# Kernel tuning notes

Measured on AMD Instinct MI355X. Metric: run time of the kernel, lower is better.

The kernel has to match this reference:

```python
import jax, jax.numpy as jnp
import numpy as np

N_NODES = 100000
N_EDGES = 800000
IN_DIM, HID, OUT_DIM = 128, 96, 32
BN_EPS = 1e-5


def gcn_conv(x, W, b, src, dst, n):
    # PyG GCNConv: linear -> symmetric-normalized aggregation (with self-loops) -> +bias
    h = x @ W  # [N, out]
    sl = jnp.arange(n)
    s = jnp.concatenate([src, sl])
    d = jnp.concatenate([dst, sl])
    deg = jax.ops.segment_sum(jnp.ones(s.shape[0], dtype=x.dtype), d, num_segments=n)
    dinv = jnp.where(deg > 0, jax.lax.rsqrt(deg), 0.0)
    norm = dinv[s] * dinv[d]  # [E+N]
    out = jax.ops.segment_sum(norm[:, None] * h[s], d, num_segments=n)
    return out + b


def batchnorm(x, gamma, beta):
    mu = jnp.mean(x, axis=0)
    var = jnp.var(x, axis=0)
    return gamma * (x - mu) * jax.lax.rsqrt(var + BN_EPS) + beta


def setup_inputs() -> dict:
    key = jax.random.key(0)
    ks = jax.random.split(key, 8)
    glorot = lambda k, fi, fo: jax.random.normal(k, (fi, fo), jnp.float32) * np.sqrt(2.0 / (fi + fo))
    return {
        "x": jax.random.normal(ks[0], (N_NODES, IN_DIM), jnp.float32),
        "edge_index": jax.random.randint(ks[1], (2, N_EDGES), 0, N_NODES, jnp.int64),
        "W1": glorot(ks[2], IN_DIM, HID), "b1": jnp.zeros((HID,), jnp.float32),
        "W2": glorot(ks[3], HID, HID), "b2": jnp.zeros((HID,), jnp.float32),
        "W3": glorot(ks[4], HID, OUT_DIM), "b3": jnp.zeros((OUT_DIM,), jnp.float32),
        "g1": jnp.ones((HID,), jnp.float32), "be1": jnp.zeros((HID,), jnp.float32),
        "g2": jnp.ones((HID,), jnp.float32), "be2": jnp.zeros((HID,), jnp.float32),
    }


def reference(x, edge_index, W1, b1, W2, b2, W3, b3, g1, be1, g2, be2):
    src, dst = edge_index[0], edge_index[1]
    n = x.shape[0]
    h = gcn_conv(x, W1, b1, src, dst, n)
    h = jax.nn.relu(batchnorm(h, g1, be1))  # dropout is identity in eval
    h = gcn_conv(h, W2, b2, src, dst, n)
    h = jax.nn.relu(batchnorm(h, g2, be2))
    h = gcn_conv(h, W3, b3, src, dst, n)
    return jax.nn.log_softmax(h, axis=-1)
```

## Files before the change

### kernel.cpp

```cpp
#include <hip/hip_runtime.h>
#include <hip/hip_fp16.h>
#include <cstddef>

#define NN 100000
#define NE 800000
#define DIN 128
#define HID 96
#define DOUT 32
static constexpr float BN_EPS = 1e-5f;
#define SCAN_NB ((NN + 255) / 256)

typedef unsigned short u16;
typedef unsigned int u32;

using f32x4 = __attribute__((ext_vector_type(4))) float;
using bf16x8 = __attribute__((ext_vector_type(8))) short;

__device__ __forceinline__ float b2f(u32 lo16) {
    union { u32 u; float f; } c; c.u = lo16 << 16; return c.f;
}
__device__ __forceinline__ u16 f2b(float f) {
    union { float f; u32 u; } c; c.f = f;
    return (u16)((c.u + 0x7FFFu + ((c.u >> 16) & 1u)) >> 16);
}
__device__ __forceinline__ u32 pack_edge(int s, float w) {
    __half h = __float2half(w);
    return ((u32)s << 15) | (u32)__half_as_ushort(h);
}
__device__ __forceinline__ int edge_src(u32 pk) { return (int)(pk >> 15); }
__device__ __forceinline__ float edge_wt(u32 pk) {
    return __half2float(__ushort_as_half((u16)(pk & 0x7FFFu)));
}


__global__ void k_init(int* __restrict__ deg) {
    int i = blockIdx.x * 256 + threadIdx.x;
    if (i < NN) deg[i] = 0;
}

__global__ __launch_bounds__(256) void k_wpack(const float* __restrict__ W1,
                                               const float* __restrict__ W2,
                                               const float* __restrict__ W3,
                                               u16* __restrict__ w1p,
                                               u16* __restrict__ w2p,
                                               u16* __restrict__ w3p) {
    int e = blockIdx.x * 256 + threadIdx.x;
    const float* W; u16* P; int N, nf, idx;
    if (e < 12288)      { W = W1; P = w1p; N = 96; nf = 24; idx = e; }
    else if (e < 21504) { W = W2; P = w2p; N = 96; nf = 18; idx = e - 12288; }
    else                { W = W3; P = w3p; N = 32; nf = 6;  idx = e - 21504; }
    int f = idx >> 9, r = idx & 511;
    int lane = r >> 3, j = r & 7;
    int CFT = N / 16;
    int kt = f / CFT, c = f % CFT;
    int k = kt * 32 + (lane >> 4) * 8 + j;
    int col = c * 16 + (lane & 15);
    float v = W[k * N + col];
    u16 hi = f2b(v);
    u16 lo = f2b(v - b2f(hi));
    P[idx] = hi;
    P[nf * 512 + idx] = lo;
}

__global__ __launch_bounds__(256) void k_scan1(const int* __restrict__ deg,
                                               int* __restrict__ row_start,
                                               int* __restrict__ blksum,
                                               float* __restrict__ dinv) {
    __shared__ int lds[256];
    int t = threadIdx.x;
    int i = blockIdx.x * 256 + t;
    int v = (i < NN) ? deg[i] : 0;
    if (i < NN) dinv[i] = rsqrtf((float)(v + 1));
    lds[t] = v;
    __syncthreads();
#pragma unroll
    for (int off = 1; off < 256; off <<= 1) {
        int add = (t >= off) ? lds[t - off] : 0;
        __syncthreads();
        lds[t] += add;
        __syncthreads();
    }
    if (i < NN) row_start[i] = lds[t] - v;
    if (t == 255) blksum[blockIdx.x] = lds[255];
}

__global__ __launch_bounds__(512) void k_scan2(int* __restrict__ blksum,
                                               int* __restrict__ row_start,
                                               float* __restrict__ meta) {
    __shared__ int lds[512];
    int t = threadIdx.x;
    if (t < 384) meta[t] = 0.f;
    int v = (t < SCAN_NB) ? blksum[t] : 0;
    lds[t] = v;
    __syncthreads();
#pragma unroll
    for (int off = 1; off < 512; off <<= 1) {
        int add = (t >= off) ? lds[t - off] : 0;
        __syncthreads();
        lds[t] += add;
        __syncthreads();
    }
    if (t < SCAN_NB) blksum[t] = lds[t] - v;
    if (t == 511) row_start[NN] = lds[511];
}

__global__ __launch_bounds__(256) void k_scan3(int* __restrict__ row_start,
                                               const int* __restrict__ blksum) {
    int i = blockIdx.x * 256 + threadIdx.x;
    if (i < NN) row_start[i] += blksum[blockIdx.x];
}

__global__ void k_scatter(const int* __restrict__ src, const int* __restrict__ dst,
                          const int* __restrict__ row_start,
                          const int* __restrict__ rank,
                          const float* __restrict__ dinv,
                          u32* __restrict__ ewt) {
    int e = blockIdx.x * blockDim.x + threadIdx.x;
    if (e < NE) {
        int d = dst[e];
        int p = row_start[d] + rank[e];
        int s = src[e];
        ewt[p] = pack_edge(s, dinv[s]);
    }
}

template <int K, int N, bool FUSE, typename XT>
__device__ __forceinline__ void gemmM_body(int bid, const XT* __restrict__ X,
                                           const u16* __restrict__ Wp,
                                           u16* __restrict__ Z,
                                           const float* __restrict__ bnA,
                                           const float* __restrict__ bnC, int M) {
    constexpr int KT = K / 32;
    constexpr int CFT = N / 16;
    constexpr int WN = (N == 96) ? 2 : 1;
    constexpr int WM = 4 / WN;
    constexpr int CF = CFT / WN;
    constexpr int RF = 64 / (WM * 16);
    constexpr int XSB = K + 8;
    __shared__ u16 Ah[64 * XSB];
    __shared__ u16 Al[64 * XSB];
    __shared__ float As[FUSE ? K : 1], Cs[FUSE ? K : 1];

    int tid = threadIdx.x;
    if (FUSE) {
        if (tid < K) { As[tid] = bnA[tid]; Cs[tid] = bnC[tid]; }
        __syncthreads();
    }
    int row0 = bid * 64;
    int sr = tid >> 2, sq = tid & 3;
    int grow = row0 + sr;
    if constexpr (sizeof(XT) == 4) {
#pragma unroll
        for (int i = 0; i < 8; ++i) {
            int c0 = sq * 32 + i * 4;
            float4 v = make_float4(0.f, 0.f, 0.f, 0.f);
            if (grow < M) v = *(const float4*)&X[(size_t)grow * K + c0];
            float vv[4] = {v.x, v.y, v.z, v.w};
            u32 hpk[2], lpk[2];
#pragma unroll
            for (int p = 0; p < 2; ++p) {
                u16 h0 = f2b(vv[2 * p]), h1 = f2b(vv[2 * p + 1]);
                u16 l0 = f2b(vv[2 * p] - b2f(h0));
                u16 l1 = f2b(vv[2 * p + 1] - b2f(h1));
                hpk[p] = (u32)h0 | ((u32)h1 << 16);
                lpk[p] = (u32)l0 | ((u32)l1 << 16);
            }
            *(uint2*)&Ah[sr * XSB + c0] = make_uint2(hpk[0], hpk[1]);
            *(uint2*)&Al[sr * XSB + c0] = make_uint2(lpk[0], lpk[1]);
        }
    } else {
#pragma unroll
        for (int i = 0; i < 3; ++i) {
            int c0 = sq * 24 + i * 8;
            uint4 v = make_uint4(0, 0, 0, 0);
            if (grow < M) v = *(const uint4*)&X[(size_t)grow * K + c0];
            u32 w[4] = {v.x, v.y, v.z, v.w};
            u32 hq[4], lq[4];
#pragma unroll
            for (int p = 0; p < 4; ++p) {
                float x0 = b2f(w[p] & 0xFFFFu);
                float x1 = b2f(w[p] >> 16);
                if (FUSE) {
                    x0 = fmaxf(fmaf(As[c0 + 2 * p], x0, Cs[c0 + 2 * p]), 0.f);
                    x1 = fmaxf(fmaf(As[c0 + 2 * p + 1], x1, Cs[c0 + 2 * p + 1]), 0.f);
                }
                u16 h0 = f2b(x0), h1 = f2b(x1);
                u16 l0 = f2b(x0 - b2f(h0)), l1 = f2b(x1 - b2f(h1));
                hq[p] = (u32)h0 | ((u32)h1 << 16);
                lq[p] = (u32)l0 | ((u32)l1 << 16);
            }
            *(uint4*)&Ah[sr * XSB + c0] = make_uint4(hq[0], hq[1], hq[2], hq[3]);
            *(uint4*)&Al[sr * XSB + c0] = make_uint4(lq[0], lq[1], lq[2], lq[3]);
        }
    }
    __syncthreads();

    int wid = tid >> 6, lane = tid & 63;
    int wm = wid & (WM - 1), wn = wid / WM;
    int lr = lane & 15, lg = lane >> 4;
    f32x4 acc[RF][CF];
#pragma unroll
    for (int a = 0; a < RF; ++a)
#pragma unroll
        for (int b = 0; b < CF; ++b) acc[a][b] = (f32x4){0.f, 0.f, 0.f, 0.f};

    const u16* WpLo = Wp + KT * CFT * 512;
#pragma unroll
    for (int kt = 0; kt < KT; ++kt) {
        bf16x8 ah[RF], al[RF];
#pragma unroll
        for (int rf = 0; rf < RF; ++rf) {
            int row = wm * (RF * 16) + rf * 16 + lr;
            ah[rf] = *(const bf16x8*)&Ah[row * XSB + kt * 32 + lg * 8];
            al[rf] = *(const bf16x8*)&Al[row * XSB + kt * 32 + lg * 8];
        }
#pragma unroll
        for (int cf = 0; cf < CF; ++cf) {
            int f = kt * CFT + wn * CF + cf;
            bf16x8 bh = *(const bf16x8*)&Wp[f * 512 + lane * 8];
            bf16x8 bl = *(const bf16x8*)&WpLo[f * 512 + lane * 8];
#pragma unroll
            for (int rf = 0; rf < RF; ++rf) {
                acc[rf][cf] = __builtin_amdgcn_mfma_f32_16x16x32_bf16(ah[rf], bh, acc[rf][cf], 0, 0, 0);
                acc[rf][cf] = __builtin_amdgcn_mfma_f32_16x16x32_bf16(al[rf], bh, acc[rf][cf], 0, 0, 0);
                acc[rf][cf] = __builtin_amdgcn_mfma_f32_16x16x32_bf16(ah[rf], bl, acc[rf][cf], 0, 0, 0);
            }
        }
    }
#pragma unroll
    for (int rf = 0; rf < RF; ++rf)
#pragma unroll
        for (int cf = 0; cf < CF; ++cf)
#pragma unroll
            for (int rr = 0; rr < 4; ++rr) {
                int gr = row0 + wm * (RF * 16) + rf * 16 + lg * 4 + rr;
                if (gr < M) {
                    int col = (wn * CF + cf) * 16 + lr;
                    Z[(size_t)gr * N + col] = f2b(acc[rf][cf][rr]);
                }
            }
}

template <int K, int N, bool FUSE, typename XT>
__global__ __launch_bounds__(256) void k_gemm(const XT* __restrict__ X,
                                              const u16* __restrict__ Wp,
                                              u16* __restrict__ Z,
                                              const float* __restrict__ bnA,
                                              const float* __restrict__ bnC, int M) {
    gemmM_body<K, N, FUSE, XT>(blockIdx.x, X, Wp, Z, bnA, bnC, M);
}

__global__ __launch_bounds__(256) void k_gemm1_hist(const float* __restrict__ X,
                                                    const u16* __restrict__ Wp,
                                                    u16* __restrict__ Z, int M,
                                                    int gemm_blocks,
                                                    const int* __restrict__ dst,
                                                    int* __restrict__ deg,
                                                    int* __restrict__ rank) {
    if ((int)blockIdx.x < gemm_blocks) {
        gemmM_body<DIN, HID, false, float>(blockIdx.x, X, Wp, Z, nullptr, nullptr, M);
    } else {
        int e = ((int)blockIdx.x - gemm_blocks) * 256 + (int)threadIdx.x;
        if (e < NE) rank[e] = atomicAdd(&deg[dst[e]], 1);
    }
}

#define ACC8(UB, W)                                                     \
    acc[0] = fmaf(W, b2f((UB).x & 0xFFFFu), acc[0]);                    \
    acc[1] = fmaf(W, b2f((UB).x >> 16), acc[1]);                        \
    acc[2] = fmaf(W, b2f((UB).y & 0xFFFFu), acc[2]);                    \
    acc[3] = fmaf(W, b2f((UB).y >> 16), acc[3]);                        \
    acc[4] = fmaf(W, b2f((UB).z & 0xFFFFu), acc[4]);                    \
    acc[5] = fmaf(W, b2f((UB).z >> 16), acc[5]);                        \
    acc[6] = fmaf(W, b2f((UB).w & 0xFFFFu), acc[6]);                    \
    acc[7] = fmaf(W, b2f((UB).w >> 16), acc[7]);

__global__ __launch_bounds__(256) void k_agg96(const u16* __restrict__ Z,
                                               u16* __restrict__ H,
                                               const float* __restrict__ bias,
                                               const int* __restrict__ row_start,
                                               const u32* __restrict__ ewt,
                                               const float* __restrict__ dinv,
                                               float* __restrict__ gsum,
                                               float* __restrict__ gsq) {
    __shared__ float ssum[96], ssq[96];
    int tid = threadIdx.x;
    if (tid < 96) { ssum[tid] = 0.f; ssq[tid] = 0.f; }
    __syncthreads();
    int wid = tid >> 6, lane = tid & 63;
    int r = lane >> 4;
    int jraw = lane & 15;
    int j = jraw < 12 ? jraw : 11;
    bool jact = jraw < 12;
    u32 j16 = (u32)j << 4;
    const char* zb = (const char*)Z;
    float bia[8];
#pragma unroll
    for (int k = 0; k < 8; ++k) bia[k] = bias[8 * j + k];
    float lsum[8], lsq[8];
#pragma unroll
    for (int k = 0; k < 8; ++k) { lsum[k] = 0.f; lsq[k] = 0.f; }
    const int S = gridDim.x * 4;

    int n = blockIdx.x * 4 + wid;
    int e0 = 0, e1 = 0;
    u32 pr = 0;
    if (n < NN) {
        e0 = row_start[n]; e1 = row_start[n + 1];
        if (e0 + lane < e1) pr = ewt[e0 + lane];
    }
    while (n < NN) {
        int n2 = n + S;
        int e0n = 0, e1n = 0;
        if (n2 < NN) { e0n = row_start[n2]; e1n = row_start[n2 + 1]; }
        u32 prn = 0;
        if (n2 < NN && e0n + lane < e1n) prn = ewt[e0n + lane];

        float dn = dinv[n];
        int m = e1 - e0;
        float acc[8];
        uint4 us4 = make_uint4(0, 0, 0, 0);
        if (r == 0) us4 = *(const uint4*)(zb + (u32)n * 192u + j16);
        if (r == 0) {
            acc[0] = dn * b2f(us4.x & 0xFFFFu); acc[1] = dn * b2f(us4.x >> 16);
            acc[2] = dn * b2f(us4.y & 0xFFFFu); acc[3] = dn * b2f(us4.y >> 16);
            acc[4] = dn * b2f(us4.z & 0xFFFFu); acc[5] = dn * b2f(us4.z >> 16);
            acc[6] = dn * b2f(us4.w & 0xFFFFu); acc[7] = dn * b2f(us4.w >> 16);
        } else {
#pragma unroll
            for (int k = 0; k < 8; ++k) acc[k] = 0.f;
        }

        if (m <= 16) {
            uint4 ub[4]; float wc[4];
            int nch = (m + 3) >> 2;
#pragma unroll
            for (int c = 0; c < 4; ++c) {
                if (c < nch) {
                    int e = 4 * c + r;
                    u32 pk = __shfl(pr, e < m ? e : 0);
                    wc[c] = (e < m) ? edge_wt(pk) : 0.f;
                    ub[c] = *(const uint4*)(zb + (pk >> 15) * 192u + j16);
                }
            }
#pragma unroll
            for (int c = 0; c < 4; ++c) {
                if (c < nch) { ACC8(ub[c], wc[c]); }
            }
        } else {
            for (int base = 0; base < m; base += 64) {
                u32 cw = pr;
                if (base) {
                    int idx = e0 + base + lane;
                    cw = (idx < e1) ? ewt[idx] : 0;
                }
                int lim = m - base; if (lim > 64) lim = 64;
                for (int c = 0; c < lim; c += 4) {
                    int e = c + r;
                    u32 pk = __shfl(cw, e < lim ? e : 0);
                    float w = (e < lim) ? edge_wt(pk) : 0.f;
                    uint4 ub = *(const uint4*)(zb + (pk >> 15) * 192u + j16);
                    ACC8(ub, w);
                }
            }
        }

#pragma unroll
        for (int k = 0; k < 8; ++k) {
            float v = acc[k];
            v += __shfl_xor(v, 16);
            v += __shfl_xor(v, 32);
            acc[k] = v;
        }
        if (r == 0 && jact) {
            float h[8];
#pragma unroll
            for (int k = 0; k < 8; ++k) {
                h[k] = fmaf(dn, acc[k], bia[k]);
                lsum[k] += h[k];
                lsq[k] = fmaf(h[k], h[k], lsq[k]);
            }
            uint4 o;
            o.x = (u32)f2b(h[0]) | ((u32)f2b(h[1]) << 16);
            o.y = (u32)f2b(h[2]) | ((u32)f2b(h[3]) << 16);
            o.z = (u32)f2b(h[4]) | ((u32)f2b(h[5]) << 16);
            o.w = (u32)f2b(h[6]) | ((u32)f2b(h[7]) << 16);
            *(uint4*)((char*)H + (u32)n * 192u + j16) = o;
        }
        n = n2; e0 = e0n; e1 = e1n; pr = prn;
    }
    if (r == 0 && jact) {
#pragma unroll
        for (int k = 0; k < 8; ++k) {
            atomicAdd(&ssum[8 * j + k], lsum[k]);
            atomicAdd(&ssq[8 * j + k], lsq[k]);
        }
    }
    __syncthreads();
    if (tid < 96) { atomicAdd(&gsum[tid], ssum[tid]); atomicAdd(&gsq[tid], ssq[tid]); }
}

__global__ void k_bncoef(const float* __restrict__ gsum, const float* __restrict__ gsq,
                         const float* __restrict__ g, const float* __restrict__ be,
                         float* __restrict__ bnA, float* __restrict__ bnC) {
    int c = threadIdx.x;
    if (c < 96) {
        float mean = gsum[c] * (1.f / NN);
        float var = gsq[c] * (1.f / NN) - mean * mean;
        float inv = rsqrtf(var + BN_EPS);
        float a = g[c] * inv;
        bnA[c] = a;
        bnC[c] = fmaf(-a, mean, be[c]);
    }
}

__global__ __launch_bounds__(256) void k_agg32_lsm(const u16* __restrict__ Z,
                                                   float* __restrict__ Out,
                                                   const float* __restrict__ bias,
                                                   const int* __restrict__ row_start,
                                                   const u32* __restrict__ ewt,
                                                   const float* __restrict__ dinv) {
    int tid = threadIdx.x;
    int wid = tid >> 6, lane = tid & 63;
    int g = lane >> 4, sl = lane & 15;
    const u32* zu = (const u32*)Z;
    float b0 = bias[2 * sl], b1 = bias[2 * sl + 1];
    int stride = gridDim.x * 16;
    for (int n0 = (blockIdx.x * 4 + wid) * 4; n0 < NN; n0 += stride) {
        int n = n0 + g;
        bool vn = n < NN;
        float dn = vn ? dinv[n] : 0.f;
        u32 uself = vn ? zu[(size_t)n * 16 + sl] : 0;
        float a0a = dn * b2f(uself & 0xFFFFu);
        float a1a = dn * b2f(uself >> 16);
        float a0b = 0.f, a1b = 0.f;
        int e0 = vn ? row_start[n] : 0, e1 = vn ? row_start[n + 1] : 0;
        for (int eb = e0; eb < e1; eb += 16) {
            int m = e1 - eb; if (m > 16) m = 16;
            int idx = eb + sl;
            u32 plv = (idx < e1) ? ewt[idx] : 0;
            u32 u_[16]; float w_[16];
#pragma unroll
            for (int q = 0; q < 16; ++q) {
                bool v = q < m;
                u32 pk = __shfl(plv, v ? q : 0, 16);
                w_[q] = v ? edge_wt(pk) : 0.f;
                u_[q] = zu[(size_t)edge_src(pk) * 16 + sl];
            }
#pragma unroll
            for (int q = 0; q < 16; q += 2) {
                a0a = fmaf(w_[q], b2f(u_[q] & 0xFFFFu), a0a);
                a1a = fmaf(w_[q], b2f(u_[q] >> 16), a1a);
                a0b = fmaf(w_[q + 1], b2f(u_[q + 1] & 0xFFFFu), a0b);
                a1b = fmaf(w_[q + 1], b2f(u_[q + 1] >> 16), a1b);
            }
        }
        float v0 = fmaf(dn, a0a + a0b, b0);
        float v1 = fmaf(dn, a1a + a1b, b1);
        float mx = fmaxf(v0, v1);
#pragma unroll
        for (int off = 8; off; off >>= 1) mx = fmaxf(mx, __shfl_xor(mx, off, 16));
        float ex = __expf(v0 - mx) + __expf(v1 - mx);
#pragma unroll
        for (int off = 8; off; off >>= 1) ex += __shfl_xor(ex, off, 16);
        float lse = mx + __logf(ex);
        if (vn) {
            float2 o = make_float2(v0 - lse, v1 - lse);
            *(float2*)&Out[(size_t)n * 32 + 2 * sl] = o;
        }
    }
}


extern "C" void kernel_launch(void* const* d_in, const int* in_sizes, int n_in,
                              void* d_out, int out_size, void* d_ws, size_t ws_size,
                              hipStream_t stream) {
    const float* x  = (const float*)d_in[0];
    const int* ei   = (const int*)d_in[1];
    const float* W1 = (const float*)d_in[2];
    const float* b1 = (const float*)d_in[3];
    const float* W2 = (const float*)d_in[4];
    const float* b2 = (const float*)d_in[5];
    const float* W3 = (const float*)d_in[6];
    const float* b3 = (const float*)d_in[7];
    const float* g1 = (const float*)d_in[8];
    const float* be1 = (const float*)d_in[9];
    const float* g2 = (const float*)d_in[10];
    const float* be2 = (const float*)d_in[11];
    float* out = (float*)d_out;

    const int* src = ei;
    const int* dst = ei + NE;

    char* p = (char*)d_ws;
    size_t off = 0;
    auto take = [&](size_t bytes) {
        char* r = p + off;
        off = (off + bytes + 255) & ~(size_t)255;
        return r;
    };
    float* dinv      = (float*)take(NN * 4);
    int*   deg       = (int*)take(NN * 4);
    int*   row_start = (int*)take((NN + 1) * 4);
    int*   blksum    = (int*)take(SCAN_NB * 4);
    int*   rank      = (int*)take((size_t)NE * 4);
    u32*   ewt       = (u32*)take((size_t)NE * 4);
    float* meta      = (float*)take(768 * 4);
    u16*   w1p       = (u16*)take(24 * 512 * 2 * 2);
    u16*   w2p       = (u16*)take(18 * 512 * 2 * 2);
    u16*   w3p       = (u16*)take(6 * 512 * 2 * 2);
    u16*   bufA      = (u16*)take((size_t)NN * HID * 2);
    u16*   bufB      = (u16*)take((size_t)NN * HID * 2);

    float* sum1 = meta + 0,   *sq1 = meta + 96;
    float* sum2 = meta + 192, *sq2 = meta + 288;
    float* bnA1 = meta + 384, *bnC1 = meta + 480;
    float* bnA2 = meta + 576, *bnC2 = meta + 672;

    const int EB = (NE + 255) / 256;
    const int VB = (NN + 255) / 256;
    const int MB = (NN + 63) / 64;
    const int AB = 2048;

    k_wpack<<<96, 256, 0, stream>>>(W1, W2, W3, w1p, w2p, w3p);
    k_init<<<VB, 256, 0, stream>>>(deg);
    k_gemm1_hist<<<MB + EB, 256, 0, stream>>>(x, w1p, bufA, NN, MB, dst, deg, rank);
    k_scan1<<<SCAN_NB, 256, 0, stream>>>(deg, row_start, blksum, dinv);
    k_scan2<<<1, 512, 0, stream>>>(blksum, row_start, meta);
    k_scan3<<<SCAN_NB, 256, 0, stream>>>(row_start, blksum);
    k_scatter<<<EB, 256, 0, stream>>>(src, dst, row_start, rank, dinv, ewt);

    k_agg96<<<AB, 256, 0, stream>>>(bufA, bufB, b1, row_start, ewt, dinv, sum1, sq1);
    k_bncoef<<<1, 128, 0, stream>>>(sum1, sq1, g1, be1, bnA1, bnC1);

    k_gemm<HID, HID, true, u16><<<MB, 256, 0, stream>>>(bufB, w2p, bufA, bnA1, bnC1, NN);
    k_agg96<<<AB, 256, 0, stream>>>(bufA, bufB, b2, row_start, ewt, dinv, sum2, sq2);
    k_bncoef<<<1, 128, 0, stream>>>(sum2, sq2, g2, be2, bnA2, bnC2);

    k_gemm<HID, DOUT, true, u16><<<MB, 256, 0, stream>>>(bufB, w3p, bufA, bnA2, bnC2, NN);
    k_agg32_lsm<<<AB, 256, 0, stream>>>(bufA, out, b3, row_start, ewt, dinv);

    (void)in_sizes; (void)n_in; (void)out_size; (void)ws_size;
}
```

Measured before the change: 384.6 us.

## Fold BN coefficient kernels into GEMMs, memset inits, restructure agg32 per-wave node

Removes the two single-block BN coefficient kernels and has each fused GEMM block compute the scale and shift from the global sums. Replaces the degree-init kernel and the meta zeroing with hipMemsetAsync calls. Rewrites the final aggregation plus log-softmax so one wave handles one node: 16 edge groups of 4 lanes each load 16-byte rows, then a cross-lane reduction follows. This cuts launch count and changes the gather pattern, at the cost of redundant coefficient math per block and more shuffle reductions.

```diff
diff --git a/kernel.cpp b/kernel.cpp
--- a/kernel.cpp
+++ b/kernel.cpp
@@ -32,11 +32,6 @@
     return __half2float(__ushort_as_half((u16)(pk & 0x7FFFu)));
 }
 
-
-__global__ void k_init(int* __restrict__ deg) {
-    int i = blockIdx.x * 256 + threadIdx.x;
-    if (i < NN) deg[i] = 0;
-}
 
 __global__ __launch_bounds__(256) void k_wpack(const float* __restrict__ W1,
                                                const float* __restrict__ W2,
@@ -85,11 +80,9 @@
 }
 
 __global__ __launch_bounds__(512) void k_scan2(int* __restrict__ blksum,
-                                               int* __restrict__ row_start,
-                                               float* __restrict__ meta) {
+                                               int* __restrict__ row_start) {
     __shared__ int lds[512];
     int t = threadIdx.x;
-    if (t < 384) meta[t] = 0.f;
     int v = (t < SCAN_NB) ? blksum[t] : 0;
     lds[t] = v;
     __syncthreads();
@@ -128,8 +121,10 @@
 __device__ __forceinline__ void gemmM_body(int bid, const XT* __restrict__ X,
                                            const u16* __restrict__ Wp,
                                            u16* __restrict__ Z,
-                                           const float* __restrict__ bnA,
-                                           const float* __restrict__ bnC, int M) {
+                                           const float* __restrict__ gsum,
+                                           const float* __restrict__ gsq,
+                                           const float* __restrict__ gam,
+                                           const float* __restrict__ bet, int M) {
     constexpr int KT = K / 32;
     constexpr int CFT = N / 16;
     constexpr int WN = (N == 96) ? 2 : 1;
@@ -143,7 +138,14 @@
 
     int tid = threadIdx.x;
     if (FUSE) {
-        if (tid < K) { As[tid] = bnA[tid]; Cs[tid] = bnC[tid]; }
+        if (tid < K) {
+            float mean = gsum[tid] * (1.f / NN);
+            float var = gsq[tid] * (1.f / NN) - mean * mean;
+            float inv = rsqrtf(var + BN_EPS);
+            float a = gam[tid] * inv;
+            As[tid] = a;
+            Cs[tid] = fmaf(-a, mean, bet[tid]);
+        }
         __syncthreads();
     }
     int row0 = bid * 64;
@@ -245,9 +247,11 @@
 __global__ __launch_bounds__(256) void k_gemm(const XT* __restrict__ X,
                                               const u16* __restrict__ Wp,
                                               u16* __restrict__ Z,
-                                              const float* __restrict__ bnA,
-                                              const float* __restrict__ bnC, int M) {
-    gemmM_body<K, N, FUSE, XT>(blockIdx.x, X, Wp, Z, bnA, bnC, M);
+                                              const float* __restrict__ gsum,
+                                              const float* __restrict__ gsq,
+                                              const float* __restrict__ gam,
+                                              const float* __restrict__ bet, int M) {
+    gemmM_body<K, N, FUSE, XT>(blockIdx.x, X, Wp, Z, gsum, gsq, gam, bet, M);
 }
 
 __global__ __launch_bounds__(256) void k_gemm1_hist(const float* __restrict__ X,
@@ -258,7 +262,8 @@
                                                     int* __restrict__ deg,
                                                     int* __restrict__ rank) {
     if ((int)blockIdx.x < gemm_blocks) {
-        gemmM_body<DIN, HID, false, float>(blockIdx.x, X, Wp, Z, nullptr, nullptr, M);
+        gemmM_body<DIN, HID, false, float>(blockIdx.x, X, Wp, Z,
+                                           nullptr, nullptr, nullptr, nullptr, M);
     } else {
         int e = ((int)blockIdx.x - gemm_blocks) * 256 + (int)threadIdx.x;
         if (e < NE) rank[e] = atomicAdd(&deg[dst[e]], 1);
@@ -400,20 +405,6 @@
     if (tid < 96) { atomicAdd(&gsum[tid], ssum[tid]); atomicAdd(&gsq[tid], ssq[tid]); }
 }
 
-__global__ void k_bncoef(const float* __restrict__ gsum, const float* __restrict__ gsq,
-                         const float* __restrict__ g, const float* __restrict__ be,
-                         float* __restrict__ bnA, float* __restrict__ bnC) {
-    int c = threadIdx.x;
-    if (c < 96) {
-        float mean = gsum[c] * (1.f / NN);
-        float var = gsq[c] * (1.f / NN) - mean * mean;
-        float inv = rsqrtf(var + BN_EPS);
-        float a = g[c] * inv;
-        bnA[c] = a;
-        bnC[c] = fmaf(-a, mean, be[c]);
-    }
-}
-
 __global__ __launch_bounds__(256) void k_agg32_lsm(const u16* __restrict__ Z,
                                                    float* __restrict__ Out,
                                                    const float* __restrict__ bias,
@@ -422,51 +413,84 @@
                                                    const float* __restrict__ dinv) {
     int tid = threadIdx.x;
     int wid = tid >> 6, lane = tid & 63;
-    int g = lane >> 4, sl = lane & 15;
-    const u32* zu = (const u32*)Z;
-    float b0 = bias[2 * sl], b1 = bias[2 * sl + 1];
-    int stride = gridDim.x * 16;
-    for (int n0 = (blockIdx.x * 4 + wid) * 4; n0 < NN; n0 += stride) {
-        int n = n0 + g;
-        bool vn = n < NN;
-        float dn = vn ? dinv[n] : 0.f;
-        u32 uself = vn ? zu[(size_t)n * 16 + sl] : 0;
-        float a0a = dn * b2f(uself & 0xFFFFu);
-        float a1a = dn * b2f(uself >> 16);
-        float a0b = 0.f, a1b = 0.f;
-        int e0 = vn ? row_start[n] : 0, e1 = vn ? row_start[n + 1] : 0;
-        for (int eb = e0; eb < e1; eb += 16) {
-            int m = e1 - eb; if (m > 16) m = 16;
-            int idx = eb + sl;
-            u32 plv = (idx < e1) ? ewt[idx] : 0;
-            u32 u_[16]; float w_[16];
-#pragma unroll
-            for (int q = 0; q < 16; ++q) {
-                bool v = q < m;
-                u32 pk = __shfl(plv, v ? q : 0, 16);
-                w_[q] = v ? edge_wt(pk) : 0.f;
-                u_[q] = zu[(size_t)edge_src(pk) * 16 + sl];
-            }
-#pragma unroll
-            for (int q = 0; q < 16; q += 2) {
-                a0a = fmaf(w_[q], b2f(u_[q] & 0xFFFFu), a0a);
-                a1a = fmaf(w_[q], b2f(u_[q] >> 16), a1a);
-                a0b = fmaf(w_[q + 1], b2f(u_[q + 1] & 0xFFFFu), a0b);
-                a1b = fmaf(w_[q + 1], b2f(u_[q + 1] >> 16), a1b);
-            }
-        }
-        float v0 = fmaf(dn, a0a + a0b, b0);
-        float v1 = fmaf(dn, a1a + a1b, b1);
-        float mx = fmaxf(v0, v1);
-#pragma unroll
-        for (int off = 8; off; off >>= 1) mx = fmaxf(mx, __shfl_xor(mx, off, 16));
-        float ex = __expf(v0 - mx) + __expf(v1 - mx);
-#pragma unroll
-        for (int off = 8; off; off >>= 1) ex += __shfl_xor(ex, off, 16);
+    int r = lane >> 2;
+    int j = lane & 3;
+    u32 j16 = (u32)j << 4;
+    const char* zb = (const char*)Z;
+    float bia[8];
+#pragma unroll
+    for (int k = 0; k < 8; ++k) bia[k] = bias[8 * j + k];
+    const int S = gridDim.x * 4;
+
+    for (int n = blockIdx.x * 4 + wid; n < NN; n += S) {
+        int e0 = row_start[n], e1 = row_start[n + 1];
+        int m = e1 - e0;
+        u32 pw = (e0 + lane < e1) ? ewt[e0 + lane] : 0;
+        float dn = dinv[n];
+        float acc[8];
+        uint4 sf = make_uint4(0, 0, 0, 0);
+        if (r == 0) sf = *(const uint4*)(zb + (u32)n * 64u + j16);
+        if (r == 0) {
+            acc[0] = dn * b2f(sf.x & 0xFFFFu); acc[1] = dn * b2f(sf.x >> 16);
+            acc[2] = dn * b2f(sf.y & 0xFFFFu); acc[3] = dn * b2f(sf.y >> 16);
+            acc[4] = dn * b2f(sf.z & 0xFFFFu); acc[5] = dn * b2f(sf.z >> 16);
+            acc[6] = dn * b2f(sf.w & 0xFFFFu); acc[7] = dn * b2f(sf.w >> 16);
+        } else {
+#pragma unroll
+            for (int k = 0; k < 8; ++k) acc[k] = 0.f;
+        }
+        int lim64 = m < 64 ? m : 64;
+        for (int base = 0; base < lim64; base += 16) {
+            int e = base + r;
+            u32 pk = __shfl(pw, e < lim64 ? e : 0);
+            float w = (e < lim64) ? edge_wt(pk) : 0.f;
+            uint4 gq = *(const uint4*)(zb + (pk >> 15) * 64u + j16);
+            ACC8(gq, w);
+        }
+        if (m > 64) {
+            for (int base = 64; base < m; base += 64) {
+                int idx = e0 + base + lane;
+                u32 cw = (idx < e1) ? ewt[idx] : 0;
+                int lim = m - base; if (lim > 64) lim = 64;
+                for (int c = 0; c < lim; c += 16) {
+                    int e = c + r;
+                    u32 pk = __shfl(cw, e < lim ? e : 0);
+                    float w = (e < lim) ? edge_wt(pk) : 0.f;
+                    uint4 gq = *(const uint4*)(zb + (pk >> 15) * 64u + j16);
+                    ACC8(gq, w);
+                }
+            }
+        }
+#pragma unroll
+        for (int k = 0; k < 8; ++k) {
+            float v = acc[k];
+            v += __shfl_xor(v, 4);
+            v += __shfl_xor(v, 8);
+            v += __shfl_xor(v, 16);
+            v += __shfl_xor(v, 32);
+            acc[k] = v;
+        }
+        float h[8];
+        float mx = -1e30f;
+#pragma unroll
+        for (int k = 0; k < 8; ++k) {
+            h[k] = fmaf(dn, acc[k], bia[k]);
+            mx = fmaxf(mx, h[k]);
+        }
+        mx = fmaxf(mx, __shfl_xor(mx, 1));
+        mx = fmaxf(mx, __shfl_xor(mx, 2));
+        float ex = 0.f;
+#pragma unroll
+        for (int k = 0; k < 8; ++k) ex += __expf(h[k] - mx);
+        ex += __shfl_xor(ex, 1);
+        ex += __shfl_xor(ex, 2);
         float lse = mx + __logf(ex);
-        if (vn) {
-            float2 o = make_float2(v0 - lse, v1 - lse);
-            *(float2*)&Out[(size_t)n * 32 + 2 * sl] = o;
+        if (r == 0) {
+            float4 o0 = make_float4(h[0] - lse, h[1] - lse, h[2] - lse, h[3] - lse);
+            float4 o1 = make_float4(h[4] - lse, h[5] - lse, h[6] - lse, h[7] - lse);
+            float* dst = &Out[(size_t)n * 32 + 8 * j];
+            *(float4*)dst = o0;
+            *(float4*)(dst + 4) = o1;
         }
     }
 }
@@ -514,30 +538,26 @@
 
     float* sum1 = meta + 0,   *sq1 = meta + 96;
     float* sum2 = meta + 192, *sq2 = meta + 288;
-    float* bnA1 = meta + 384, *bnC1 = meta + 480;
-    float* bnA2 = meta + 576, *bnC2 = meta + 672;
 
     const int EB = (NE + 255) / 256;
-    const int VB = (NN + 255) / 256;
     const int MB = (NN + 63) / 64;
     const int AB = 2048;
 
+    hipMemsetAsync(deg, 0, NN * 4, stream);
+    hipMemsetAsync(meta, 0, 768 * 4, stream);
     k_wpack<<<96, 256, 0, stream>>>(W1, W2, W3, w1p, w2p, w3p);
-    k_init<<<VB, 256, 0, stream>>>(deg);
     k_gemm1_hist<<<MB + EB, 256, 0, stream>>>(x, w1p, bufA, NN, MB, dst, deg, rank);
     k_scan1<<<SCAN_NB, 256, 0, stream>>>(deg, row_start, blksum, dinv);
-    k_scan2<<<1, 512, 0, stream>>>(blksum, row_start, meta);
+    k_scan2<<<1, 512, 0, stream>>>(blksum, row_start);
     k_scan3<<<SCAN_NB, 256, 0, stream>>>(row_start, blksum);
     k_scatter<<<EB, 256, 0, stream>>>(src, dst, row_start, rank, dinv, ewt);
 
     k_agg96<<<AB, 256, 0, stream>>>(bufA, bufB, b1, row_start, ewt, dinv, sum1, sq1);
-    k_bncoef<<<1, 128, 0, stream>>>(sum1, sq1, g1, be1, bnA1, bnC1);
-
-    k_gemm<HID, HID, true, u16><<<MB, 256, 0, stream>>>(bufB, w2p, bufA, bnA1, bnC1, NN);
+
+    k_gemm<HID, HID, true, u16><<<MB, 256, 0, stream>>>(bufB, w2p, bufA, sum1, sq1, g1, be1, NN);
     k_agg96<<<AB, 256, 0, stream>>>(bufA, bufB, b2, row_start, ewt, dinv, sum2, sq2);
-    k_bncoef<<<1, 128, 0, stream>>>(sum2, sq2, g2, be2, bnA2, bnC2);
-
-    k_gemm<HID, DOUT, true, u16><<<MB, 256, 0, stream>>>(bufB, w3p, bufA, bnA2, bnC2, NN);
+
+    k_gemm<HID, DOUT, true, u16><<<MB, 256, 0, stream>>>(bufB, w3p, bufA, sum2, sq2, g2, be2, NN);
     k_agg32_lsm<<<AB, 256, 0, stream>>>(bufA, out, b3, row_start, ewt, dinv);
 
     (void)in_sizes; (void)n_in; (void)out_size; (void)ws_size;
```

Result: slower. 412.0 us (+7.1%).
